# Kernel optimization log

Measured on AMD Instinct MI355X. Metric: run time of the kernel, lower is better.

## Reference

```python
import jax, jax.numpy as jnp
import numpy as np

B, N, M, D, OUT, K = 8, 32, 64, 128, 128, 3
EPS = 1e-5


def batchnorm(x, g, b):
    # training-mode BatchNorm2d over NCHW (stats over B,H,W per channel, biased var)
    mean = x.mean((0, 2, 3), keepdims=True)
    var = ((x - mean) ** 2).mean((0, 2, 3), keepdims=True)
    return g[None, :, None, None] * (x - mean) * jax.lax.rsqrt(var + EPS) + b[None, :, None, None]


def mycorr(x):
    # Pearson correlation between nodes along feature dim: x (B,M,N,D) -> (B,M,N,N)
    xc = x - x.mean(-1, keepdims=True)
    num = jnp.einsum('bmid,bmjd->bmij', xc, xc)
    nrm = jnp.sqrt((xc * xc).sum(-1))
    return num / (nrm[:, :, :, None] * nrm[:, :, None, :] + 1e-8)


def attention(x, W_fc1, W_fc2):
    # x: (B,M,N,D). AdaptiveAvgPool2d((None,1)) over the concat [Wh_i, pos*Wh_j]
    # equals 0.5*(mean_d Wh_i + mean_d(pos*Wh_j)); pos=1 where Wh_i==Wh_j else 2.
    adj = mycorr(x)
    mean_i = x.mean(-1)                       # (B,M,N)
    xi = x[:, :, :, None, :]                  # (B,M,N,1,D)
    xj = x[:, :, None, :, :]                  # (B,M,1,N,D)
    alt_mean = jnp.where(xi == xj, xj, 2.0 * xj).mean(-1)  # (B,M,N,N)
    e = 0.5 * (mean_i[:, :, :, None] + alt_mean)            # (B,M,N,N)
    ef = e.reshape(e.shape[0], e.shape[1], -1)              # (B,M,N*N) pair channels
    h = jax.nn.relu(jnp.einsum('rp,bmp->bmr', W_fc1, ef))
    e2 = jax.nn.sigmoid(jnp.einsum('pr,bmr->bmp', W_fc2, h)).reshape(e.shape)
    att = jax.nn.softmax(jnp.where(adj > 0, e2, jnp.float32(-1e12)), axis=-1)
    return jnp.einsum('bmij,bmjd->bmid', att, x)


def setup_inputs() -> dict:
    key = jax.random.key(0)
    ks = jax.random.split(key, 8)
    P, r, s = N * N, (N * N) // 2, 0.05
    return {
        'x': jax.random.normal(ks[0], (B, N, M, D), jnp.float32),
        'W_sc': jax.random.normal(ks[1], (OUT, M), jnp.float32) * s,
        'g_sc': jnp.ones(OUT, jnp.float32), 'b_sc': jnp.zeros(OUT, jnp.float32),
        'W_l1': jax.random.normal(ks[2], (M, M), jnp.float32) * s,
        'g1': jnp.ones(M, jnp.float32), 'b1': jnp.zeros(M, jnp.float32),
        'W_fc1': jax.random.normal(ks[3], (r, P), jnp.float32) * s,
        'W_fc2': jax.random.normal(ks[4], (P, r), jnp.float32) * s,
        'g2': jnp.ones(M, jnp.float32), 'b2': jnp.zeros(M, jnp.float32),
        'W_dw': jax.random.normal(ks[5], (N, 1, K, K), jnp.float32) * s,
        'g3': jnp.ones(N, jnp.float32), 'b3': jnp.zeros(N, jnp.float32),
        'W_l3': jax.random.normal(ks[6], (OUT, M), jnp.float32) * s,
    }


def reference(x, W_sc, g_sc, b_sc, W_l1, g1, b1, W_fc1, W_fc2, g2, b2, W_dw, g3, b3, W_l3):
    xm = jnp.transpose(x, (0, 2, 1, 3))  # (B,M,N,D)
    # shortcut: 1x1 conv over head channel + BN (stride=1 path)
    shortcut = batchnorm(jnp.einsum('om,bmnd->bond', W_sc, xm), g_sc, b_sc)
    # layer_1: 1x1 conv, BN, global node attention, BN, ReLU
    out = batchnorm(jnp.einsum('cm,bmnd->bcnd', W_l1, xm), g1, b1)
    out = attention(out, W_fc1, W_fc2)
    out = jax.nn.relu(batchnorm(out, g2, b2))
    # layer_2: depthwise KxK conv over (head, dim) per node, BN, ReLU
    out = jnp.transpose(out, (0, 2, 1, 3))  # (B,N,M,D)
    pad = K // 2
    out = jax.lax.conv_general_dilated(out, W_dw, (1, 1), ((pad, pad), (pad, pad)),
                                       feature_group_count=N,
                                       dimension_numbers=('NCHW', 'OIHW', 'NCHW'))
    out = jax.nn.relu(batchnorm(out, g3, b3))
    # layer_3: 1x1 conv to out_channels heads + residual
    out = jnp.transpose(out, (0, 2, 1, 3))  # (B,M,N,D)
    out = jnp.einsum('om,bmnd->bond', W_l3, out) + shortcut
    return jnp.transpose(out, (0, 2, 1, 3))  # (B,N,OUT,D)
```

## Files before the change

### kernel.cpp

```cpp
#include <hip/hip_runtime.h>
#include <math.h>

#define EPS 1e-5f


__device__ __forceinline__ void fma4(float4& a, float s, const float4& v) {
    a.x += s * v.x; a.y += s * v.y; a.z += s * v.z; a.w += s * v.w;
}

__global__ __launch_bounds__(256) void k1_matmul_stats(
    const float* __restrict__ x, const float* __restrict__ Wsc,
    const float* __restrict__ Wl1, const float* __restrict__ Wfc1,
    float* __restrict__ t_sc, float* __restrict__ t_l1,
    float* __restrict__ C1, float* __restrict__ stats)
{
    int g  = blockIdx.x;
    int bn = blockIdx.y;
    __shared__ __align__(16) float s_x[64 * 128];
    __shared__ __align__(16) float s_wT[64 * 68];
    int t = threadIdx.x;

    if (g == 3) {
#pragma unroll
        for (int rr = 0; rr < 2; rr++) {
            int r = bn * 2 + rr;
            *(float4*)(s_x + t * 4) =
                *(const float4*)(Wfc1 + (size_t)r * 1024 + t * 4);
            __syncthreads();
            if (t < 32) {
                float rs = 0.f, cs = 0.f;
#pragma unroll
                for (int j = 0; j < 32; j++) {
                    rs += s_x[t * 32 + j];
                    cs += s_x[j * 32 + t];
                }
                C1[r * 32 + t] = (rs + 2.f * cs - s_x[t * 33]) * (1.0f / 256.0f);
            }
            __syncthreads();
        }
        return;
    }

    int b = bn >> 5, n = bn & 31;
    const float4* xg = (const float4*)(x + (size_t)bn * 8192);
    for (int i = t; i < 2048; i += 256) ((float4*)s_x)[i] = xg[i];

    const float* wbase = (g < 2) ? (Wsc + (size_t)g * 64 * 64) : Wl1;
    for (int i = t; i < 1024; i += 256) {
        int m = i >> 4, rq = (i & 15) * 4;
        float4 wv;
        wv.x = wbase[(size_t)(rq + 0) * 64 + m];
        wv.y = wbase[(size_t)(rq + 1) * 64 + m];
        wv.z = wbase[(size_t)(rq + 2) * 64 + m];
        wv.w = wbase[(size_t)(rq + 3) * 64 + m];
        *(float4*)(s_wT + m * 68 + rq) = wv;
    }
    __syncthreads();

    int wv = t >> 6, lane = t & 63;
    int dl = lane & 15;
    int g4 = lane >> 4;
    int d0 = dl * 8;
    int c0 = wv * 16 + g4 * 4;

    float4 acc[4][2];
#pragma unroll
    for (int i = 0; i < 4; i++) { acc[i][0] = make_float4(0,0,0,0); acc[i][1] = make_float4(0,0,0,0); }

    for (int m = 0; m < 64; m += 2) {
        float4 x00 = *(const float4*)(s_x + m * 128 + d0);
        float4 x01 = *(const float4*)(s_x + m * 128 + d0 + 4);
        float4 x10 = *(const float4*)(s_x + (m + 1) * 128 + d0);
        float4 x11 = *(const float4*)(s_x + (m + 1) * 128 + d0 + 4);
        float4 w0 = *(const float4*)(s_wT + m * 68 + c0);
        float4 w1 = *(const float4*)(s_wT + (m + 1) * 68 + c0);
        fma4(acc[0][0], w0.x, x00); fma4(acc[0][1], w0.x, x01);
        fma4(acc[1][0], w0.y, x00); fma4(acc[1][1], w0.y, x01);
        fma4(acc[2][0], w0.z, x00); fma4(acc[2][1], w0.z, x01);
        fma4(acc[3][0], w0.w, x00); fma4(acc[3][1], w0.w, x01);
        fma4(acc[0][0], w1.x, x10); fma4(acc[0][1], w1.x, x11);
        fma4(acc[1][0], w1.y, x10); fma4(acc[1][1], w1.y, x11);
        fma4(acc[2][0], w1.z, x10); fma4(acc[2][1], w1.z, x11);
        fma4(acc[3][0], w1.w, x10); fma4(acc[3][1], w1.w, x11);
    }

#pragma unroll
    for (int i = 0; i < 4; i++) {
        int cc = g * 64 + c0 + i;
        float4 v0 = acc[i][0], v1 = acc[i][1];
        float* dst;
        if (cc < 128) dst = t_sc + (((size_t)(b * 128 + cc)) * 32 + n) * 128 + d0;
        else          dst = t_l1 + (((size_t)(b * 64 + (cc - 128))) * 32 + n) * 128 + d0;
        *(float4*)dst = v0;
        *(float4*)(dst + 4) = v1;
        float s = v0.x + v0.y + v0.z + v0.w + v1.x + v1.y + v1.z + v1.w;
        float q = v0.x*v0.x + v0.y*v0.y + v0.z*v0.z + v0.w*v0.w
                + v1.x*v1.x + v1.y*v1.y + v1.z*v1.z + v1.w*v1.w;
#pragma unroll
        for (int off = 8; off > 0; off >>= 1) {
            s += __shfl_down(s, off, 16);
            q += __shfl_down(q, off, 16);
        }
        if (dl == 0) {
            if (cc < 128) {
                atomicAdd(&stats[cc], s);
                atomicAdd(&stats[cc + 128], q);
            } else {
                atomicAdd(&stats[256 + (cc - 128)], s);
                atomicAdd(&stats[320 + (cc - 128)], q);
            }
        }
    }
}

__global__ __launch_bounds__(256) void k2_attn_prep(
    const float* __restrict__ t_l1, const float* __restrict__ g1,
    const float* __restrict__ b1, const float* __restrict__ stats,
    const float* __restrict__ Wfc1, const float* __restrict__ C1,
    float* __restrict__ y_g, float* __restrict__ H,
    unsigned int* __restrict__ maskbits)
{
    int bm = blockIdx.x;
    int t  = threadIdx.x;
    __shared__ __align__(16) float y_s[32 * 132];
    __shared__ float S_s[32];
    __shared__ unsigned int m_s[32];
    __shared__ int anom_cnt;
    __shared__ int anom_p[64];
    __shared__ float anom_v[64];
    int m = bm & 63;
    float mean = stats[256 + m] * (1.0f / 32768.0f);
    float var  = stats[320 + m] * (1.0f / 32768.0f) - mean * mean;
    float a = g1[m] * rsqrtf(var + EPS);
    float c = b1[m] - a * mean;

    if (t == 0) anom_cnt = 0;
    if (t < 32) m_s[t] = 0u;
    const float4* src = (const float4*)(t_l1 + (size_t)bm * 4096);
    for (int i = t; i < 1024; i += 256) {
        float4 v = src[i];
        v.x = a * v.x + c; v.y = a * v.y + c; v.z = a * v.z + c; v.w = a * v.w + c;
        int row = i >> 5, col = (i & 31) * 4;
        *(float4*)(y_s + row * 132 + col) = v;
    }
    __syncthreads();

    {
        int r = t >> 3, j = t & 7;
        float s = 0.f;
        const float* yr = y_s + r * 132 + j * 16;
#pragma unroll
        for (int dd = 0; dd < 16; dd++) s += yr[dd];
#pragma unroll
        for (int off = 4; off > 0; off >>= 1) s += __shfl_down(s, off, 8);
        if (j == 0) S_s[r] = s;
    }
    __syncthreads();

    int i = t >> 3, j0 = (t & 7) * 4;
    float dot[4] = {0.f, 0.f, 0.f, 0.f};
    float eqs[4] = {0.f, 0.f, 0.f, 0.f};
    const float* yi = y_s + i * 132;
    for (int dq = 0; dq < 32; dq++) {
        float4 a4 = *(const float4*)(yi + dq * 4);
#pragma unroll
        for (int q = 0; q < 4; q++) {
            float4 b4 = *(const float4*)(y_s + (j0 + q) * 132 + dq * 4);
            dot[q] += a4.x * b4.x + a4.y * b4.y + a4.z * b4.z + a4.w * b4.w;
            eqs[q] += (a4.x == b4.x ? b4.x : 0.f) + (a4.y == b4.y ? b4.y : 0.f)
                    + (a4.z == b4.z ? b4.z : 0.f) + (a4.w == b4.w ? b4.w : 0.f);
        }
    }
    float Si = S_s[i];
    unsigned int bits = 0u;
#pragma unroll
    for (int q = 0; q < 4; q++) {
        int j = j0 + q;
        float Sj = S_s[j];
        float num = dot[q] - Si * Sj * (1.0f / 128.0f);
        if (num > 0.f) bits |= (1u << j);
        if (j != i && eqs[q] != 0.f) {
            int idx = atomicAdd(&anom_cnt, 1);
            if (idx < 64) {
                anom_p[idx] = i * 32 + j;
                anom_v[idx] = eqs[q] * (1.0f / 256.0f);
            }
        }
    }
    atomicOr(&m_s[i], bits);
    __syncthreads();
    if (t < 32) maskbits[bm * 32 + t] = m_s[t];

    int cnt = anom_cnt; if (cnt > 64) cnt = 64;
#pragma unroll
    for (int rr = 0; rr < 2; rr++) {
        int r = t * 2 + rr;
        const float4* c1r = (const float4*)(C1 + r * 32);
        float acc = 0.f;
#pragma unroll
        for (int kk = 0; kk < 8; kk++) {
            float4 cv = c1r[kk];
            acc += cv.x * S_s[kk * 4 + 0] + cv.y * S_s[kk * 4 + 1]
                 + cv.z * S_s[kk * 4 + 2] + cv.w * S_s[kk * 4 + 3];
        }
        for (int a2 = 0; a2 < cnt; a2++)
            acc -= Wfc1[(size_t)r * 1024 + anom_p[a2]] * anom_v[a2];
        H[(size_t)bm * 512 + r] = fmaxf(acc, 0.f);
    }

    float4* yd = (float4*)(y_g + (size_t)bm * 4096);
    for (int idx = t; idx < 1024; idx += 256) {
        int row = idx >> 5, col = (idx & 31) * 4;
        yd[idx] = *(const float4*)(y_s + row * 132 + col);
    }
}

template<int KDIM, int MODE>
__global__ __launch_bounds__(256) void k3_gemm(
    const float* __restrict__ A, const float* __restrict__ Bm,
    float* __restrict__ C, int NC)
{
    __shared__ __align__(16) float lds[4 * 2304];
    int t = threadIdx.x;
    int w = t >> 6, l = t & 63;
    int ct = blockIdx.x, rt = blockIdx.y;
    int row0 = rt * 32, col0 = ct * 32;
    float* As = lds + w * 2304;
    float* Bs = As + 1152;
    int rg = l >> 3;
    int cg = l & 7;
    int kq = (l & 7) * 4;
    constexpr int SLABS = KDIM / 128;

    float4 acc[4];
#pragma unroll
    for (int ii = 0; ii < 4; ii++) acc[ii] = make_float4(0,0,0,0);

    float4 av[4], bv[4], av2[4], bv2[4];
    int k0 = w * 32;
#pragma unroll
    for (int rr = 0; rr < 4; rr++) {
        int r = rg + rr * 8;
        av[rr] = *(const float4*)(A  + (size_t)(row0 + r) * KDIM + k0 + kq);
        bv[rr] = *(const float4*)(Bm + (size_t)(col0 + r) * KDIM + k0 + kq);
    }

    for (int s = 0; s < SLABS; s++) {
#pragma unroll
        for (int rr = 0; rr < 4; rr++) {
            int r = rg + rr * 8;
            As[(kq + 0) * 36 + r] = av[rr].x; As[(kq + 1) * 36 + r] = av[rr].y;
            As[(kq + 2) * 36 + r] = av[rr].z; As[(kq + 3) * 36 + r] = av[rr].w;
            Bs[(kq + 0) * 36 + r] = bv[rr].x; Bs[(kq + 1) * 36 + r] = bv[rr].y;
            Bs[(kq + 2) * 36 + r] = bv[rr].z; Bs[(kq + 3) * 36 + r] = bv[rr].w;
        }
        if (s + 1 < SLABS) {
            int kn = (4 * (s + 1) + w) * 32;
#pragma unroll
            for (int rr = 0; rr < 4; rr++) {
                int r = rg + rr * 8;
                av2[rr] = *(const float4*)(A  + (size_t)(row0 + r) * KDIM + kn + kq);
                bv2[rr] = *(const float4*)(Bm + (size_t)(col0 + r) * KDIM + kn + kq);
            }
        }
#pragma unroll
        for (int k = 0; k < 32; k++) {
            float4 a = *(const float4*)(As + k * 36 + rg * 4);
            float4 b = *(const float4*)(Bs + k * 36 + cg * 4);
            fma4(acc[0], a.x, b);
            fma4(acc[1], a.y, b);
            fma4(acc[2], a.z, b);
            fma4(acc[3], a.w, b);
        }
#pragma unroll
        for (int rr = 0; rr < 4; rr++) { av[rr] = av2[rr]; bv[rr] = bv2[rr]; }
    }

    __syncthreads();
    float* red = lds;
#pragma unroll
    for (int ii = 0; ii < 4; ii++)
        *(float4*)(red + w * 1024 + (rg * 4 + ii) * 32 + cg * 4) = acc[ii];
    __syncthreads();

    int r = t >> 3, c4 = (t & 7) * 4;
    float4 s0 = *(const float4*)(red + r * 32 + c4);
    float4 s1 = *(const float4*)(red + 1024 + r * 32 + c4);
    float4 s2 = *(const float4*)(red + 2048 + r * 32 + c4);
    float4 s3 = *(const float4*)(red + 3072 + r * 32 + c4);
    float4 v;
    v.x = s0.x + s1.x + s2.x + s3.x;
    v.y = s0.y + s1.y + s2.y + s3.y;
    v.z = s0.z + s1.z + s2.z + s3.z;
    v.w = s0.w + s1.w + s2.w + s3.w;
    if (MODE == 0) {
        v.x = fmaxf(v.x, 0.f); v.y = fmaxf(v.y, 0.f);
        v.z = fmaxf(v.z, 0.f); v.w = fmaxf(v.w, 0.f);
    } else {
        v.x = 1.0f / (1.0f + expf(-v.x)); v.y = 1.0f / (1.0f + expf(-v.y));
        v.z = 1.0f / (1.0f + expf(-v.z)); v.w = 1.0f / (1.0f + expf(-v.w));
    }
    *(float4*)(C + (size_t)(row0 + r) * NC + col0 + c4) = v;
}

__global__ __launch_bounds__(256) void k4_attn_apply(
    const float* __restrict__ E2, const unsigned int* __restrict__ maskbits,
    const float* __restrict__ y_g, float* __restrict__ att_out,
    float* __restrict__ stats)
{
    int bm = blockIdx.x;
    int t  = threadIdx.x;
    __shared__ __align__(16) float att_s[32 * 33];
    __shared__ __align__(16) float y_sh[32 * 128];
    __shared__ float redS[4], redQ[4];

    const float4* ysrc = (const float4*)(y_g + (size_t)bm * 4096);
    float4* yds = (float4*)y_sh;
    for (int i = t; i < 1024; i += 256) yds[i] = ysrc[i];

    {
        int r = t >> 3, j0 = (t & 7) * 4;
        unsigned int mk = maskbits[bm * 32 + r];
        float4 e4 = *(const float4*)(E2 + (size_t)bm * 1024 + r * 32 + j0);
        float v0 = ((mk >> (j0 + 0)) & 1u) ? e4.x : -1e12f;
        float v1 = ((mk >> (j0 + 1)) & 1u) ? e4.y : -1e12f;
        float v2 = ((mk >> (j0 + 2)) & 1u) ? e4.z : -1e12f;
        float v3 = ((mk >> (j0 + 3)) & 1u) ? e4.w : -1e12f;
        float mx = fmaxf(fmaxf(v0, v1), fmaxf(v2, v3));
#pragma unroll
        for (int off = 1; off < 8; off <<= 1) mx = fmaxf(mx, __shfl_xor(mx, off, 8));
        float e0 = __expf(v0 - mx), e1 = __expf(v1 - mx);
        float e2 = __expf(v2 - mx), e3 = __expf(v3 - mx);
        float s = e0 + e1 + e2 + e3;
#pragma unroll
        for (int off = 1; off < 8; off <<= 1) s += __shfl_xor(s, off, 8);
        float inv = 1.0f / s;
        att_s[r * 33 + j0 + 0] = e0 * inv;
        att_s[r * 33 + j0 + 1] = e1 * inv;
        att_s[r * 33 + j0 + 2] = e2 * inv;
        att_s[r * 33 + j0 + 3] = e3 * inv;
    }
    __syncthreads();

    int tx = t & 31, ty = t >> 5;
    int dq = tx * 4;
    int i0 = ty * 4;
    float4 acc0 = make_float4(0,0,0,0), acc1 = make_float4(0,0,0,0);
    float4 acc2 = make_float4(0,0,0,0), acc3 = make_float4(0,0,0,0);
    for (int j = 0; j < 32; j++) {
        float4 yv = *(const float4*)(y_sh + j * 128 + dq);
        float w0 = att_s[(i0 + 0) * 33 + j];
        float w1 = att_s[(i0 + 1) * 33 + j];
        float w2 = att_s[(i0 + 2) * 33 + j];
        float w3 = att_s[(i0 + 3) * 33 + j];
        fma4(acc0, w0, yv);
        fma4(acc1, w1, yv);
        fma4(acc2, w2, yv);
        fma4(acc3, w3, yv);
    }
    float ssum = 0.f, sq = 0.f;
    float4 accs[4] = {acc0, acc1, acc2, acc3};
#pragma unroll
    for (int ii = 0; ii < 4; ii++) {
        float4 acc = accs[ii];
        *(float4*)(att_out + (size_t)bm * 4096 + (i0 + ii) * 128 + dq) = acc;
        ssum += acc.x + acc.y + acc.z + acc.w;
        sq   += acc.x * acc.x + acc.y * acc.y + acc.z * acc.z + acc.w * acc.w;
    }
#pragma unroll
    for (int off = 32; off > 0; off >>= 1) {
        ssum += __shfl_down(ssum, off, 64);
        sq   += __shfl_down(sq, off, 64);
    }
    int wave = t >> 6, lane = t & 63;
    if (lane == 0) { redS[wave] = ssum; redQ[wave] = sq; }
    __syncthreads();
    if (t == 0) {
        float S = redS[0] + redS[1] + redS[2] + redS[3];
        float Q = redQ[0] + redQ[1] + redQ[2] + redQ[3];
        int m = bm & 63;
        atomicAdd(&stats[384 + m], S);
        atomicAdd(&stats[448 + m], Q);
    }
}

__global__ __launch_bounds__(256) void k5_conv(
    const float* __restrict__ att_out, const float* __restrict__ Wdw,
    const float* __restrict__ g2, const float* __restrict__ b2,
    float* __restrict__ stats, float* __restrict__ v_g)
{
    int bn = blockIdx.x;
    int b = bn >> 5, n = bn & 31;
    int t = threadIdx.x;
    __shared__ __align__(16) float z_s[66 * 130];
    __shared__ float a2_s[64], c2_s[64];
    __shared__ float redS[4], redQ[4];

    if (t < 64) {
        float mean = stats[384 + t] * (1.0f / 32768.0f);
        float var  = stats[448 + t] * (1.0f / 32768.0f) - mean * mean;
        float a = g2[t] * rsqrtf(var + EPS);
        a2_s[t] = a; c2_s[t] = b2[t] - a * mean;
    }
    for (int i = t; i < 66 * 130; i += 256) z_s[i] = 0.f;
    __syncthreads();

    for (int i = t; i < 2048; i += 256) {
        int m = i >> 5, c4 = (i & 31) * 4;
        float4 vv = *(const float4*)(att_out + (((size_t)(b * 64 + m)) * 32 + n) * 128 + c4);
        float a = a2_s[m], c = c2_s[m];
        float* dst = z_s + (m + 1) * 130 + c4 + 1;
        dst[0] = fmaxf(a * vv.x + c, 0.f);
        dst[1] = fmaxf(a * vv.y + c, 0.f);
        dst[2] = fmaxf(a * vv.z + c, 0.f);
        dst[3] = fmaxf(a * vv.w + c, 0.f);
    }
    float w[9];
#pragma unroll
    for (int i = 0; i < 9; i++) w[i] = Wdw[n * 9 + i];
    __syncthreads();

    int tx = t & 31, ty = t >> 5;
    int d0 = tx * 4;
    float ssum = 0.f, sq = 0.f;
#pragma unroll
    for (int rr = 0; rr < 8; rr++) {
        int h = ty * 8 + rr;
        float o0 = 0.f, o1 = 0.f, o2 = 0.f, o3 = 0.f;
#pragma unroll
        for (int dh = 0; dh < 3; dh++) {
            const float* zr = z_s + (h + dh) * 130 + d0;
#pragma unroll
            for (int dw = 0; dw < 3; dw++) {
                float wv = w[dh * 3 + dw];
                o0 += wv * zr[dw + 0];
                o1 += wv * zr[dw + 1];
                o2 += wv * zr[dw + 2];
                o3 += wv * zr[dw + 3];
            }
        }
        *(float4*)(v_g + ((size_t)bn * 64 + h) * 128 + d0) = make_float4(o0, o1, o2, o3);
        ssum += o0 + o1 + o2 + o3;
        sq   += o0 * o0 + o1 * o1 + o2 * o2 + o3 * o3;
    }
#pragma unroll
    for (int off = 32; off > 0; off >>= 1) {
        ssum += __shfl_down(ssum, off, 64);
        sq   += __shfl_down(sq, off, 64);
    }
    int wave = t >> 6, lane = t & 63;
    if (lane == 0) { redS[wave] = ssum; redQ[wave] = sq; }
    __syncthreads();
    if (t == 0) {
        atomicAdd(&stats[512 + n], redS[0] + redS[1] + redS[2] + redS[3]);
        atomicAdd(&stats[544 + n], redQ[0] + redQ[1] + redQ[2] + redQ[3]);
    }
}

__global__ __launch_bounds__(256) void k6_final(
    const float* __restrict__ v_g, const float* __restrict__ t_sc,
    const float* __restrict__ Wl3, const float* __restrict__ g3,
    const float* __restrict__ b3, const float* __restrict__ gsc,
    const float* __restrict__ bsc, const float* __restrict__ stats,
    float* __restrict__ outp)
{
    int oh = blockIdx.x;
    int bn = blockIdx.y;
    int b = bn >> 5, n = bn & 31;
    int t = threadIdx.x;
    __shared__ __align__(16) float z_s[64 * 128];
    __shared__ __align__(16) float s_wT[64 * 68];

    float mean3 = stats[512 + n] * (1.0f / 65536.0f);
    float var3  = stats[544 + n] * (1.0f / 65536.0f) - mean3 * mean3;
    float a3 = g3[n] * rsqrtf(var3 + EPS);
    float c3 = b3[n] - a3 * mean3;

    const float4* vsrc = (const float4*)(v_g + (size_t)bn * 8192);
    for (int i = t; i < 2048; i += 256) {
        float4 vv = vsrc[i];
        float4 r;
        r.x = fmaxf(a3 * vv.x + c3, 0.f);
        r.y = fmaxf(a3 * vv.y + c3, 0.f);
        r.z = fmaxf(a3 * vv.z + c3, 0.f);
        r.w = fmaxf(a3 * vv.w + c3, 0.f);
        ((float4*)z_s)[i] = r;
    }
    const float* wbase = Wl3 + (size_t)oh * 64 * 64;
    for (int i = t; i < 1024; i += 256) {
        int m = i >> 4, rq = (i & 15) * 4;
        float4 wv;
        wv.x = wbase[(size_t)(rq + 0) * 64 + m];
        wv.y = wbase[(size_t)(rq + 1) * 64 + m];
        wv.z = wbase[(size_t)(rq + 2) * 64 + m];
        wv.w = wbase[(size_t)(rq + 3) * 64 + m];
        *(float4*)(s_wT + m * 68 + rq) = wv;
    }
    __syncthreads();

    int wv = t >> 6, lane = t & 63;
    int dl = lane & 15, g4 = lane >> 4;
    int d0 = dl * 8;
    int c0 = wv * 16 + g4 * 4;

    float4 acc[4][2];
#pragma unroll
    for (int i = 0; i < 4; i++) { acc[i][0] = make_float4(0,0,0,0); acc[i][1] = make_float4(0,0,0,0); }

    for (int m = 0; m < 64; m += 2) {
        float4 x00 = *(const float4*)(z_s + m * 128 + d0);
        float4 x01 = *(const float4*)(z_s + m * 128 + d0 + 4);
        float4 x10 = *(const float4*)(z_s + (m + 1) * 128 + d0);
        float4 x11 = *(const float4*)(z_s + (m + 1) * 128 + d0 + 4);
        float4 w0 = *(const float4*)(s_wT + m * 68 + c0);
        float4 w1 = *(const float4*)(s_wT + (m + 1) * 68 + c0);
        fma4(acc[0][0], w0.x, x00); fma4(acc[0][1], w0.x, x01);
        fma4(acc[1][0], w0.y, x00); fma4(acc[1][1], w0.y, x01);
        fma4(acc[2][0], w0.z, x00); fma4(acc[2][1], w0.z, x01);
        fma4(acc[3][0], w0.w, x00); fma4(acc[3][1], w0.w, x01);
        fma4(acc[0][0], w1.x, x10); fma4(acc[0][1], w1.x, x11);
        fma4(acc[1][0], w1.y, x10); fma4(acc[1][1], w1.y, x11);
        fma4(acc[2][0], w1.z, x10); fma4(acc[2][1], w1.z, x11);
        fma4(acc[3][0], w1.w, x10); fma4(acc[3][1], w1.w, x11);
    }

#pragma unroll
    for (int i = 0; i < 4; i++) {
        int o = oh * 64 + c0 + i;
        float msc = stats[o] * (1.0f / 32768.0f);
        float vsc = stats[128 + o] * (1.0f / 32768.0f) - msc * msc;
        float asc = gsc[o] * rsqrtf(vsc + EPS);
        float csc = bsc[o] - asc * msc;
        const float* ts = t_sc + (((size_t)(b * 128 + o)) * 32 + n) * 128 + d0;
        float4 t0 = *(const float4*)(ts);
        float4 t1 = *(const float4*)(ts + 4);
        float4 o0 = acc[i][0], o1 = acc[i][1];
        o0.x += asc * t0.x + csc; o0.y += asc * t0.y + csc;
        o0.z += asc * t0.z + csc; o0.w += asc * t0.w + csc;
        o1.x += asc * t1.x + csc; o1.y += asc * t1.y + csc;
        o1.z += asc * t1.z + csc; o1.w += asc * t1.w + csc;
        float* dst = outp + (((size_t)(b * 32 + n)) * 128 + o) * 128 + d0;
        *(float4*)dst = o0;
        *(float4*)(dst + 4) = o1;
    }
}

extern "C" void kernel_launch(void* const* d_in, const int* in_sizes, int n_in,
                              void* d_out, int out_size, void* d_ws, size_t ws_size,
                              hipStream_t stream)
{
    const float* x    = (const float*)d_in[0];
    const float* Wsc  = (const float*)d_in[1];
    const float* gsc  = (const float*)d_in[2];
    const float* bsc  = (const float*)d_in[3];
    const float* Wl1  = (const float*)d_in[4];
    const float* g1   = (const float*)d_in[5];
    const float* b1   = (const float*)d_in[6];
    const float* Wfc1 = (const float*)d_in[7];
    const float* Wfc2 = (const float*)d_in[8];
    const float* g2   = (const float*)d_in[9];
    const float* b2   = (const float*)d_in[10];
    const float* Wdw  = (const float*)d_in[11];
    const float* g3   = (const float*)d_in[12];
    const float* b3   = (const float*)d_in[13];
    const float* Wl3  = (const float*)d_in[14];
    float* outp = (float*)d_out;

    float* ws = (float*)d_ws;
    float* stats = ws;
    float* t_sc  = ws + 1024;
    float* t_l1  = t_sc + 4194304;
    float* y_g   = t_l1 + 2097152;
    float* C1    = y_g + 2097152;
    float* H     = C1 + 16384;
    float* E2    = H + 262144;
    unsigned int* maskb = (unsigned int*)(E2 + 524288);

    (void)hipMemsetAsync(stats, 0, 1024 * sizeof(float), stream);

    k1_matmul_stats<<<dim3(4, 256), 256, 0, stream>>>(x, Wsc, Wl1, Wfc1, t_sc, t_l1, C1, stats);
    k2_attn_prep<<<512, 256, 0, stream>>>(t_l1, g1, b1, stats, Wfc1, C1, y_g, H, maskb);
    k3_gemm<512, 1><<<dim3(32, 16), 256, 0, stream>>>(H, Wfc2, E2, 1024);
    k4_attn_apply<<<512, 256, 0, stream>>>(E2, maskb, y_g, t_l1, stats);
    k5_conv<<<256, 256, 0, stream>>>(t_l1, Wdw, g2, b2, stats, y_g);
    k6_final<<<dim3(2, 256), 256, 0, stream>>>(y_g, t_sc, Wl3, g3, b3, gsc, bsc, stats, outp);
}
```

Measured before the change: 198.8 us.

## Retile 1x1-conv kernels with split-K register tiles and padded shared layouts

The k1 and k6 1x1-conv GEMMs now give each thread an 8-channel by 8-element register tile. The 64-wide reduction is split across two wave pairs, and the halves are combined through shared memory before the epilogue. The x/z and attention y tiles get padded shared-memory strides to cut bank conflicts, and weight transposition loads are restructured to coalesce. The point is to raise FMA-to-LDS ratio and reduce bank conflicts. The cost is higher register pressure (launch_bounds 256,3), an extra shared-memory reduction with two syncs, and half the waves idle in the epilogue.

```diff
diff --git a/kernel.cpp b/kernel.cpp
--- a/kernel.cpp
+++ b/kernel.cpp
@@ -8,7 +8,17 @@
     a.x += s * v.x; a.y += s * v.y; a.z += s * v.z; a.w += s * v.w;
 }
 
-__global__ __launch_bounds__(256) void k1_matmul_stats(
+#define FMA_STEP(W0, W1, X0, X1) \
+    fma4(acc[0][0], W0.x, X0); fma4(acc[0][1], W0.x, X1); \
+    fma4(acc[1][0], W0.y, X0); fma4(acc[1][1], W0.y, X1); \
+    fma4(acc[2][0], W0.z, X0); fma4(acc[2][1], W0.z, X1); \
+    fma4(acc[3][0], W0.w, X0); fma4(acc[3][1], W0.w, X1); \
+    fma4(acc[4][0], W1.x, X0); fma4(acc[4][1], W1.x, X1); \
+    fma4(acc[5][0], W1.y, X0); fma4(acc[5][1], W1.y, X1); \
+    fma4(acc[6][0], W1.z, X0); fma4(acc[6][1], W1.z, X1); \
+    fma4(acc[7][0], W1.w, X0); fma4(acc[7][1], W1.w, X1);
+
+__global__ __launch_bounds__(256, 3) void k1_matmul_stats(
     const float* __restrict__ x, const float* __restrict__ Wsc,
     const float* __restrict__ Wl1, const float* __restrict__ Wfc1,
     float* __restrict__ t_sc, float* __restrict__ t_l1,
@@ -16,7 +26,7 @@
 {
     int g  = blockIdx.x;
     int bn = blockIdx.y;
-    __shared__ __align__(16) float s_x[64 * 128];
+    __shared__ __align__(16) float s_x[64 * 144];
     __shared__ __align__(16) float s_wT[64 * 68];
     int t = threadIdx.x;
 
@@ -43,75 +53,108 @@
 
     int b = bn >> 5, n = bn & 31;
     const float4* xg = (const float4*)(x + (size_t)bn * 8192);
-    for (int i = t; i < 2048; i += 256) ((float4*)s_x)[i] = xg[i];
-
-    const float* wbase = (g < 2) ? (Wsc + (size_t)g * 64 * 64) : Wl1;
-    for (int i = t; i < 1024; i += 256) {
-        int m = i >> 4, rq = (i & 15) * 4;
-        float4 wv;
-        wv.x = wbase[(size_t)(rq + 0) * 64 + m];
-        wv.y = wbase[(size_t)(rq + 1) * 64 + m];
-        wv.z = wbase[(size_t)(rq + 2) * 64 + m];
-        wv.w = wbase[(size_t)(rq + 3) * 64 + m];
-        *(float4*)(s_wT + m * 68 + rq) = wv;
-    }
-    __syncthreads();
-
-    int wv = t >> 6, lane = t & 63;
-    int dl = lane & 15;
-    int g4 = lane >> 4;
+    for (int i = t; i < 2048; i += 256) {
+        int row = i >> 5, j = i & 31;
+        *(float4*)(s_x + row * 144 + j * 4 + ((j >> 3) << 2)) = xg[i];
+    }
+    const float* wbase = (g < 2) ? (Wsc + (size_t)g * 4096) : Wl1;
+    {
+        int m = t & 63, tg = t >> 6;
+        float val[16];
+#pragma unroll
+        for (int o = 0; o < 16; o++)
+            val[o] = wbase[(size_t)(tg * 16 + o) * 64 + m];
+        float* wr = s_wT + m * 68 + tg * 16;
+#pragma unroll
+        for (int q = 0; q < 8; q++)
+            *(float2*)(wr + 2 * q) = make_float2(val[2 * q], val[2 * q + 1]);
+    }
+    __syncthreads();
+
+    int w = t >> 6, lane = t & 63;
+    int mh = w >> 1, p = w & 1;
+    int dl = lane & 15, cg = lane >> 4;
     int d0 = dl * 8;
-    int c0 = wv * 16 + g4 * 4;
-
-    float4 acc[4][2];
-#pragma unroll
-    for (int i = 0; i < 4; i++) { acc[i][0] = make_float4(0,0,0,0); acc[i][1] = make_float4(0,0,0,0); }
-
-    for (int m = 0; m < 64; m += 2) {
-        float4 x00 = *(const float4*)(s_x + m * 128 + d0);
-        float4 x01 = *(const float4*)(s_x + m * 128 + d0 + 4);
-        float4 x10 = *(const float4*)(s_x + (m + 1) * 128 + d0);
-        float4 x11 = *(const float4*)(s_x + (m + 1) * 128 + d0 + 4);
-        float4 w0 = *(const float4*)(s_wT + m * 68 + c0);
-        float4 w1 = *(const float4*)(s_wT + (m + 1) * 68 + c0);
-        fma4(acc[0][0], w0.x, x00); fma4(acc[0][1], w0.x, x01);
-        fma4(acc[1][0], w0.y, x00); fma4(acc[1][1], w0.y, x01);
-        fma4(acc[2][0], w0.z, x00); fma4(acc[2][1], w0.z, x01);
-        fma4(acc[3][0], w0.w, x00); fma4(acc[3][1], w0.w, x01);
-        fma4(acc[0][0], w1.x, x10); fma4(acc[0][1], w1.x, x11);
-        fma4(acc[1][0], w1.y, x10); fma4(acc[1][1], w1.y, x11);
-        fma4(acc[2][0], w1.z, x10); fma4(acc[2][1], w1.z, x11);
-        fma4(acc[3][0], w1.w, x10); fma4(acc[3][1], w1.w, x11);
-    }
-
-#pragma unroll
-    for (int i = 0; i < 4; i++) {
-        int cc = g * 64 + c0 + i;
-        float4 v0 = acc[i][0], v1 = acc[i][1];
-        float* dst;
-        if (cc < 128) dst = t_sc + (((size_t)(b * 128 + cc)) * 32 + n) * 128 + d0;
-        else          dst = t_l1 + (((size_t)(b * 64 + (cc - 128))) * 32 + n) * 128 + d0;
-        *(float4*)dst = v0;
-        *(float4*)(dst + 4) = v1;
-        float s = v0.x + v0.y + v0.z + v0.w + v1.x + v1.y + v1.z + v1.w;
-        float q = v0.x*v0.x + v0.y*v0.y + v0.z*v0.z + v0.w*v0.w
-                + v1.x*v1.x + v1.y*v1.y + v1.z*v1.z + v1.w*v1.w;
-#pragma unroll
-        for (int off = 8; off > 0; off >>= 1) {
-            s += __shfl_down(s, off, 16);
-            q += __shfl_down(q, off, 16);
-        }
-        if (dl == 0) {
-            if (cc < 128) {
-                atomicAdd(&stats[cc], s);
-                atomicAdd(&stats[cc + 128], q);
-            } else {
-                atomicAdd(&stats[256 + (cc - 128)], s);
-                atomicAdd(&stats[320 + (cc - 128)], q);
+    int ch = p * 32 + cg * 8;
+    int xoff = d0 + ((dl >> 2) << 2);
+
+    float4 acc[8][2];
+#pragma unroll
+    for (int i = 0; i < 8; i++) { acc[i][0] = make_float4(0,0,0,0); acc[i][1] = make_float4(0,0,0,0); }
+
+    int m0 = mh * 32;
+    for (int m = m0; m < m0 + 32; m += 2) {
+        const float* xr0 = s_x + m * 144 + xoff;
+        const float* wr0 = s_wT + m * 68 + ch;
+        float4 xA0 = *(const float4*)(xr0);
+        float4 xA1 = *(const float4*)(xr0 + 4);
+        float4 xB0 = *(const float4*)(xr0 + 144);
+        float4 xB1 = *(const float4*)(xr0 + 148);
+        float4 wA0 = *(const float4*)(wr0);
+        float4 wA1 = *(const float4*)(wr0 + 4);
+        float4 wB0 = *(const float4*)(wr0 + 68);
+        float4 wB1 = *(const float4*)(wr0 + 72);
+        FMA_STEP(wA0, wA1, xA0, xA1)
+        FMA_STEP(wB0, wB1, xB0, xB1)
+    }
+
+    __syncthreads();
+    float* s_red = s_x;
+    if (mh == 1) {
+        float* row = s_red + (p * 64 + lane) * 66;
+#pragma unroll
+        for (int i = 0; i < 8; i++) {
+            *(float2*)(row + i * 8 + 0) = make_float2(acc[i][0].x, acc[i][0].y);
+            *(float2*)(row + i * 8 + 2) = make_float2(acc[i][0].z, acc[i][0].w);
+            *(float2*)(row + i * 8 + 4) = make_float2(acc[i][1].x, acc[i][1].y);
+            *(float2*)(row + i * 8 + 6) = make_float2(acc[i][1].z, acc[i][1].w);
+        }
+    }
+    __syncthreads();
+    if (mh == 0) {
+        const float* row = s_red + (p * 64 + lane) * 66;
+#pragma unroll
+        for (int i = 0; i < 8; i++) {
+            float2 p0 = *(const float2*)(row + i * 8 + 0);
+            float2 p1 = *(const float2*)(row + i * 8 + 2);
+            float2 p2 = *(const float2*)(row + i * 8 + 4);
+            float2 p3 = *(const float2*)(row + i * 8 + 6);
+            acc[i][0].x += p0.x; acc[i][0].y += p0.y;
+            acc[i][0].z += p1.x; acc[i][0].w += p1.y;
+            acc[i][1].x += p2.x; acc[i][1].y += p2.y;
+            acc[i][1].z += p3.x; acc[i][1].w += p3.y;
+        }
+#pragma unroll
+        for (int i = 0; i < 8; i++) {
+            int cc = g * 64 + ch + i;
+            float4 v0 = acc[i][0], v1 = acc[i][1];
+            float* dst;
+            if (cc < 128) dst = t_sc + (((size_t)(b * 128 + cc)) * 32 + n) * 128 + d0;
+            else          dst = t_l1 + (((size_t)(b * 64 + (cc - 128))) * 32 + n) * 128 + d0;
+            *(float4*)dst = v0;
+            *(float4*)(dst + 4) = v1;
+            float s = v0.x + v0.y + v0.z + v0.w + v1.x + v1.y + v1.z + v1.w;
+            float q = v0.x*v0.x + v0.y*v0.y + v0.z*v0.z + v0.w*v0.w
+                    + v1.x*v1.x + v1.y*v1.y + v1.z*v1.z + v1.w*v1.w;
+#pragma unroll
+            for (int off = 8; off > 0; off >>= 1) {
+                s += __shfl_down(s, off, 16);
+                q += __shfl_down(q, off, 16);
             }
-        }
-    }
-}
+            if (dl == 0) {
+                if (cc < 128) {
+                    atomicAdd(&stats[cc], s);
+                    atomicAdd(&stats[cc + 128], q);
+                } else {
+                    atomicAdd(&stats[256 + (cc - 128)], s);
+                    atomicAdd(&stats[320 + (cc - 128)], q);
+                }
+            }
+        }
+    }
+}
+
+__device__ __forceinline__ int yb(int r) { return r * 132 + ((r >> 2) << 3); }
 
 __global__ __launch_bounds__(256) void k2_attn_prep(
     const float* __restrict__ t_l1, const float* __restrict__ g1,
@@ -122,7 +165,7 @@
 {
     int bm = blockIdx.x;
     int t  = threadIdx.x;
-    __shared__ __align__(16) float y_s[32 * 132];
+    __shared__ __align__(16) float y_s[4288];
     __shared__ float S_s[32];
     __shared__ unsigned int m_s[32];
     __shared__ int anom_cnt;
@@ -141,14 +184,14 @@
         float4 v = src[i];
         v.x = a * v.x + c; v.y = a * v.y + c; v.z = a * v.z + c; v.w = a * v.w + c;
         int row = i >> 5, col = (i & 31) * 4;
-        *(float4*)(y_s + row * 132 + col) = v;
+        *(float4*)(y_s + yb(row) + col) = v;
     }
     __syncthreads();
 
     {
         int r = t >> 3, j = t & 7;
         float s = 0.f;
-        const float* yr = y_s + r * 132 + j * 16;
+        const float* yr = y_s + yb(r) + j * 16;
 #pragma unroll
         for (int dd = 0; dd < 16; dd++) s += yr[dd];
 #pragma unroll
@@ -160,12 +203,14 @@
     int i = t >> 3, j0 = (t & 7) * 4;
     float dot[4] = {0.f, 0.f, 0.f, 0.f};
     float eqs[4] = {0.f, 0.f, 0.f, 0.f};
-    const float* yi = y_s + i * 132;
+    const float* yi = y_s + yb(i);
+    const float* yj[4] = { y_s + yb(j0), y_s + yb(j0 + 1),
+                           y_s + yb(j0 + 2), y_s + yb(j0 + 3) };
     for (int dq = 0; dq < 32; dq++) {
         float4 a4 = *(const float4*)(yi + dq * 4);
 #pragma unroll
         for (int q = 0; q < 4; q++) {
-            float4 b4 = *(const float4*)(y_s + (j0 + q) * 132 + dq * 4);
+            float4 b4 = *(const float4*)(yj[q] + dq * 4);
             dot[q] += a4.x * b4.x + a4.y * b4.y + a4.z * b4.z + a4.w * b4.w;
             eqs[q] += (a4.x == b4.x ? b4.x : 0.f) + (a4.y == b4.y ? b4.y : 0.f)
                     + (a4.z == b4.z ? b4.z : 0.f) + (a4.w == b4.w ? b4.w : 0.f);
@@ -211,7 +256,7 @@
     float4* yd = (float4*)(y_g + (size_t)bm * 4096);
     for (int idx = t; idx < 1024; idx += 256) {
         int row = idx >> 5, col = (idx & 31) * 4;
-        yd[idx] = *(const float4*)(y_s + row * 132 + col);
+        yd[idx] = *(const float4*)(y_s + yb(row) + col);
     }
 }
 
@@ -457,7 +502,7 @@
     }
 }
 
-__global__ __launch_bounds__(256) void k6_final(
+__global__ __launch_bounds__(256, 3) void k6_final(
     const float* __restrict__ v_g, const float* __restrict__ t_sc,
     const float* __restrict__ Wl3, const float* __restrict__ g3,
     const float* __restrict__ b3, const float* __restrict__ gsc,
@@ -468,7 +513,7 @@
     int bn = blockIdx.y;
     int b = bn >> 5, n = bn & 31;
     int t = threadIdx.x;
-    __shared__ __align__(16) float z_s[64 * 128];
+    __shared__ __align__(16) float z_s[64 * 144];
     __shared__ __align__(16) float s_wT[64 * 68];
 
     float mean3 = stats[512 + n] * (1.0f / 65536.0f);
@@ -484,64 +529,95 @@
         r.y = fmaxf(a3 * vv.y + c3, 0.f);
         r.z = fmaxf(a3 * vv.z + c3, 0.f);
         r.w = fmaxf(a3 * vv.w + c3, 0.f);
-        ((float4*)z_s)[i] = r;
-    }
-    const float* wbase = Wl3 + (size_t)oh * 64 * 64;
-    for (int i = t; i < 1024; i += 256) {
-        int m = i >> 4, rq = (i & 15) * 4;
-        float4 wv;
-        wv.x = wbase[(size_t)(rq + 0) * 64 + m];
-        wv.y = wbase[(size_t)(rq + 1) * 64 + m];
-        wv.z = wbase[(size_t)(rq + 2) * 64 + m];
-        wv.w = wbase[(size_t)(rq + 3) * 64 + m];
-        *(float4*)(s_wT + m * 68 + rq) = wv;
-    }
-    __syncthreads();
-
-    int wv = t >> 6, lane = t & 63;
-    int dl = lane & 15, g4 = lane >> 4;
+        int row = i >> 5, j = i & 31;
+        *(float4*)(z_s + row * 144 + j * 4 + ((j >> 3) << 2)) = r;
+    }
+    const float* wbase = Wl3 + (size_t)oh * 4096;
+    {
+        int m = t & 63, tg = t >> 6;
+        float val[16];
+#pragma unroll
+        for (int o = 0; o < 16; o++)
+            val[o] = wbase[(size_t)(tg * 16 + o) * 64 + m];
+        float* wr = s_wT + m * 68 + tg * 16;
+#pragma unroll
+        for (int q = 0; q < 8; q++)
+            *(float2*)(wr + 2 * q) = make_float2(val[2 * q], val[2 * q + 1]);
+    }
+    __syncthreads();
+
+    int w = t >> 6, lane = t & 63;
+    int mh = w >> 1, p = w & 1;
+    int dl = lane & 15, cg = lane >> 4;
     int d0 = dl * 8;
-    int c0 = wv * 16 + g4 * 4;
-
-    float4 acc[4][2];
-#pragma unroll
-    for (int i = 0; i < 4; i++) { acc[i][0] = make_float4(0,0,0,0); acc[i][1] = make_float4(0,0,0,0); }
-
-    for (int m = 0; m < 64; m += 2) {
-        float4 x00 = *(const float4*)(z_s + m * 128 + d0);
-        float4 x01 = *(const float4*)(z_s + m * 128 + d0 + 4);
-        float4 x10 = *(const float4*)(z_s + (m + 1) * 128 + d0);
-        float4 x11 = *(const float4*)(z_s + (m + 1) * 128 + d0 + 4);
-        float4 w0 = *(const float4*)(s_wT + m * 68 + c0);
-        float4 w1 = *(const float4*)(s_wT + (m + 1) * 68 + c0);
-        fma4(acc[0][0], w0.x, x00); fma4(acc[0][1], w0.x, x01);
-        fma4(acc[1][0], w0.y, x00); fma4(acc[1][1], w0.y, x01);
-        fma4(acc[2][0], w0.z, x00); fma4(acc[2][1], w0.z, x01);
-        fma4(acc[3][0], w0.w, x00); fma4(acc[3][1], w0.w, x01);
-        fma4(acc[0][0], w1.x, x10); fma4(acc[0][1], w1.x, x11);
-        fma4(acc[1][0], w1.y, x10); fma4(acc[1][1], w1.y, x11);
-        fma4(acc[2][0], w1.z, x10); fma4(acc[2][1], w1.z, x11);
-        fma4(acc[3][0], w1.w, x10); fma4(acc[3][1], w1.w, x11);
-    }
-
-#pragma unroll
-    for (int i = 0; i < 4; i++) {
-        int o = oh * 64 + c0 + i;
-        float msc = stats[o] * (1.0f / 32768.0f);
-        float vsc = stats[128 + o] * (1.0f / 32768.0f) - msc * msc;
-        float asc = gsc[o] * rsqrtf(vsc + EPS);
-        float csc = bsc[o] - asc * msc;
-        const float* ts = t_sc + (((size_t)(b * 128 + o)) * 32 + n) * 128 + d0;
-        float4 t0 = *(const float4*)(ts);
-        float4 t1 = *(const float4*)(ts + 4);
-        float4 o0 = acc[i][0], o1 = acc[i][1];
-        o0.x += asc * t0.x + csc; o0.y += asc * t0.y + csc;
-        o0.z += asc * t0.z + csc; o0.w += asc * t0.w + csc;
-        o1.x += asc * t1.x + csc; o1.y += asc * t1.y + csc;
-        o1.z += asc * t1.z + csc; o1.w += asc * t1.w + csc;
-        float* dst = outp + (((size_t)(b * 32 + n)) * 128 + o) * 128 + d0;
-        *(float4*)dst = o0;
-        *(float4*)(dst + 4) = o1;
+    int ch = p * 32 + cg * 8;
+    int xoff = d0 + ((dl >> 2) << 2);
+
+    float4 acc[8][2];
+#pragma unroll
+    for (int i = 0; i < 8; i++) { acc[i][0] = make_float4(0,0,0,0); acc[i][1] = make_float4(0,0,0,0); }
+
+    int m0 = mh * 32;
+    for (int m = m0; m < m0 + 32; m += 2) {
+        const float* xr0 = z_s + m * 144 + xoff;
+        const float* wr0 = s_wT + m * 68 + ch;
+        float4 xA0 = *(const float4*)(xr0);
+        float4 xA1 = *(const float4*)(xr0 + 4);
+        float4 xB0 = *(const float4*)(xr0 + 144);
+        float4 xB1 = *(const float4*)(xr0 + 148);
+        float4 wA0 = *(const float4*)(wr0);
+        float4 wA1 = *(const float4*)(wr0 + 4);
+        float4 wB0 = *(const float4*)(wr0 + 68);
+        float4 wB1 = *(const float4*)(wr0 + 72);
+        FMA_STEP(wA0, wA1, xA0, xA1)
+        FMA_STEP(wB0, wB1, xB0, xB1)
+    }
+
+    __syncthreads();
+    float* s_red = z_s;
+    if (mh == 1) {
+        float* row = s_red + (p * 64 + lane) * 66;
+#pragma unroll
+        for (int i = 0; i < 8; i++) {
+            *(float2*)(row + i * 8 + 0) = make_float2(acc[i][0].x, acc[i][0].y);
+            *(float2*)(row + i * 8 + 2) = make_float2(acc[i][0].z, acc[i][0].w);
+            *(float2*)(row + i * 8 + 4) = make_float2(acc[i][1].x, acc[i][1].y);
+            *(float2*)(row + i * 8 + 6) = make_float2(acc[i][1].z, acc[i][1].w);
+        }
+    }
+    __syncthreads();
+    if (mh == 0) {
+        const float* row = s_red + (p * 64 + lane) * 66;
+#pragma unroll
+        for (int i = 0; i < 8; i++) {
+            float2 p0 = *(const float2*)(row + i * 8 + 0);
+            float2 p1 = *(const float2*)(row + i * 8 + 2);
+            float2 p2 = *(const float2*)(row + i * 8 + 4);
+            float2 p3 = *(const float2*)(row + i * 8 + 6);
+            acc[i][0].x += p0.x; acc[i][0].y += p0.y;
+            acc[i][0].z += p1.x; acc[i][0].w += p1.y;
+            acc[i][1].x += p2.x; acc[i][1].y += p2.y;
+            acc[i][1].z += p3.x; acc[i][1].w += p3.y;
+        }
+#pragma unroll
+        for (int i = 0; i < 8; i++) {
+            int o = oh * 64 + ch + i;
+            float msc = stats[o] * (1.0f / 32768.0f);
+            float vsc = stats[128 + o] * (1.0f / 32768.0f) - msc * msc;
+            float asc = gsc[o] * rsqrtf(vsc + EPS);
+            float csc = bsc[o] - asc * msc;
+            const float* ts = t_sc + (((size_t)(b * 128 + o)) * 32 + n) * 128 + d0;
+            float4 t0 = *(const float4*)(ts);
+            float4 t1 = *(const float4*)(ts + 4);
+            float4 o0 = acc[i][0], o1 = acc[i][1];
+            o0.x += asc * t0.x + csc; o0.y += asc * t0.y + csc;
+            o0.z += asc * t0.z + csc; o0.w += asc * t0.w + csc;
+            o1.x += asc * t1.x + csc; o1.y += asc * t1.y + csc;
+            o1.z += asc * t1.z + csc; o1.w += asc * t1.w + csc;
+            float* dst = outp + (((size_t)(b * 32 + n)) * 128 + o) * 128 + d0;
+            *(float4*)dst = o0;
+            *(float4*)(dst + 4) = o1;
+        }
     }
 }
 
```

Result: slower. 213.6 us (+7.5%).

## Pre-transpose 1x1-conv weights once and pad shared tiles to avoid bank conflicts

Applied to the files above, without the earlier changes.

Adds a small kernel that transposes the shortcut, layer-1 and layer-3 1x1-conv weights into global buffers once per call. k1 and k6 then read weights straight from global/L2 instead of each block doing strided transposes into shared memory, which cuts LDS use and allows four blocks per CU via launch bounds. Shared activation tiles get padded row strides and swizzle offsets in k1, k2 and k6 to reduce LDS bank conflicts, and the inner loops are unrolled. This costs an extra kernel launch and moves the weight reads into the inner loop, where they now hit cache rather than LDS.

```diff
diff --git a/kernel.cpp b/kernel.cpp
--- a/kernel.cpp
+++ b/kernel.cpp
@@ -8,16 +8,32 @@
     a.x += s * v.x; a.y += s * v.y; a.z += s * v.z; a.w += s * v.w;
 }
 
-__global__ __launch_bounds__(256) void k1_matmul_stats(
-    const float* __restrict__ x, const float* __restrict__ Wsc,
-    const float* __restrict__ Wl1, const float* __restrict__ Wfc1,
-    float* __restrict__ t_sc, float* __restrict__ t_l1,
-    float* __restrict__ C1, float* __restrict__ stats)
+__global__ __launch_bounds__(256) void k0_transpose(
+    const float* __restrict__ Wsc, const float* __restrict__ Wl1,
+    const float* __restrict__ Wl3, float* __restrict__ Wt,
+    float* __restrict__ Wt3)
+{
+    int idx = blockIdx.x * 256 + threadIdx.x;
+    if (idx < 12288) {
+        int m = idx / 192, cc = idx % 192;
+        Wt[idx] = (cc < 128) ? Wsc[(size_t)cc * 64 + m]
+                             : Wl1[(size_t)(cc - 128) * 64 + m];
+    } else if (idx < 20480) {
+        int k = idx - 12288;
+        int m = k >> 7, o = k & 127;
+        Wt3[k] = Wl3[(size_t)o * 64 + m];
+    }
+}
+
+__global__ __launch_bounds__(256, 4) void k1_matmul_stats(
+    const float* __restrict__ x, const float* __restrict__ Wt,
+    const float* __restrict__ Wfc1, float* __restrict__ t_sc,
+    float* __restrict__ t_l1, float* __restrict__ C1,
+    float* __restrict__ stats)
 {
     int g  = blockIdx.x;
     int bn = blockIdx.y;
-    __shared__ __align__(16) float s_x[64 * 128];
-    __shared__ __align__(16) float s_wT[64 * 68];
+    __shared__ __align__(16) float s_x[64 * 144];
     int t = threadIdx.x;
 
     if (g == 3) {
@@ -43,37 +59,32 @@
 
     int b = bn >> 5, n = bn & 31;
     const float4* xg = (const float4*)(x + (size_t)bn * 8192);
-    for (int i = t; i < 2048; i += 256) ((float4*)s_x)[i] = xg[i];
-
-    const float* wbase = (g < 2) ? (Wsc + (size_t)g * 64 * 64) : Wl1;
-    for (int i = t; i < 1024; i += 256) {
-        int m = i >> 4, rq = (i & 15) * 4;
-        float4 wv;
-        wv.x = wbase[(size_t)(rq + 0) * 64 + m];
-        wv.y = wbase[(size_t)(rq + 1) * 64 + m];
-        wv.z = wbase[(size_t)(rq + 2) * 64 + m];
-        wv.w = wbase[(size_t)(rq + 3) * 64 + m];
-        *(float4*)(s_wT + m * 68 + rq) = wv;
+    for (int i = t; i < 2048; i += 256) {
+        int row = i >> 5, j = i & 31;
+        *(float4*)(s_x + row * 144 + j * 4 + ((j >> 3) << 2)) = xg[i];
     }
     __syncthreads();
 
     int wv = t >> 6, lane = t & 63;
-    int dl = lane & 15;
-    int g4 = lane >> 4;
+    int dl = lane & 15, g4 = lane >> 4;
     int d0 = dl * 8;
     int c0 = wv * 16 + g4 * 4;
+    int xoff = d0 + ((dl >> 2) << 2);
+    const float* wt = Wt + g * 64 + c0;
 
     float4 acc[4][2];
 #pragma unroll
     for (int i = 0; i < 4; i++) { acc[i][0] = make_float4(0,0,0,0); acc[i][1] = make_float4(0,0,0,0); }
 
+#pragma unroll 4
     for (int m = 0; m < 64; m += 2) {
-        float4 x00 = *(const float4*)(s_x + m * 128 + d0);
-        float4 x01 = *(const float4*)(s_x + m * 128 + d0 + 4);
-        float4 x10 = *(const float4*)(s_x + (m + 1) * 128 + d0);
-        float4 x11 = *(const float4*)(s_x + (m + 1) * 128 + d0 + 4);
-        float4 w0 = *(const float4*)(s_wT + m * 68 + c0);
-        float4 w1 = *(const float4*)(s_wT + (m + 1) * 68 + c0);
+        const float* xr = s_x + m * 144 + xoff;
+        float4 x00 = *(const float4*)(xr);
+        float4 x01 = *(const float4*)(xr + 4);
+        float4 x10 = *(const float4*)(xr + 144);
+        float4 x11 = *(const float4*)(xr + 148);
+        float4 w0 = *(const float4*)(wt + m * 192);
+        float4 w1 = *(const float4*)(wt + (m + 1) * 192);
         fma4(acc[0][0], w0.x, x00); fma4(acc[0][1], w0.x, x01);
         fma4(acc[1][0], w0.y, x00); fma4(acc[1][1], w0.y, x01);
         fma4(acc[2][0], w0.z, x00); fma4(acc[2][1], w0.z, x01);
@@ -113,6 +124,8 @@
     }
 }
 
+__device__ __forceinline__ int yb(int r) { return r * 132 + ((r >> 2) << 3); }
+
 __global__ __launch_bounds__(256) void k2_attn_prep(
     const float* __restrict__ t_l1, const float* __restrict__ g1,
     const float* __restrict__ b1, const float* __restrict__ stats,
@@ -122,7 +135,7 @@
 {
     int bm = blockIdx.x;
     int t  = threadIdx.x;
-    __shared__ __align__(16) float y_s[32 * 132];
+    __shared__ __align__(16) float y_s[4288];
     __shared__ float S_s[32];
     __shared__ unsigned int m_s[32];
     __shared__ int anom_cnt;
@@ -141,14 +154,14 @@
         float4 v = src[i];
         v.x = a * v.x + c; v.y = a * v.y + c; v.z = a * v.z + c; v.w = a * v.w + c;
         int row = i >> 5, col = (i & 31) * 4;
-        *(float4*)(y_s + row * 132 + col) = v;
+        *(float4*)(y_s + yb(row) + col) = v;
     }
     __syncthreads();
 
     {
         int r = t >> 3, j = t & 7;
         float s = 0.f;
-        const float* yr = y_s + r * 132 + j * 16;
+        const float* yr = y_s + yb(r) + j * 16;
 #pragma unroll
         for (int dd = 0; dd < 16; dd++) s += yr[dd];
 #pragma unroll
@@ -160,12 +173,14 @@
     int i = t >> 3, j0 = (t & 7) * 4;
     float dot[4] = {0.f, 0.f, 0.f, 0.f};
     float eqs[4] = {0.f, 0.f, 0.f, 0.f};
-    const float* yi = y_s + i * 132;
+    const float* yi = y_s + yb(i);
+    const float* yj[4] = { y_s + yb(j0), y_s + yb(j0 + 1),
+                           y_s + yb(j0 + 2), y_s + yb(j0 + 3) };
     for (int dq = 0; dq < 32; dq++) {
         float4 a4 = *(const float4*)(yi + dq * 4);
 #pragma unroll
         for (int q = 0; q < 4; q++) {
-            float4 b4 = *(const float4*)(y_s + (j0 + q) * 132 + dq * 4);
+            float4 b4 = *(const float4*)(yj[q] + dq * 4);
             dot[q] += a4.x * b4.x + a4.y * b4.y + a4.z * b4.z + a4.w * b4.w;
             eqs[q] += (a4.x == b4.x ? b4.x : 0.f) + (a4.y == b4.y ? b4.y : 0.f)
                     + (a4.z == b4.z ? b4.z : 0.f) + (a4.w == b4.w ? b4.w : 0.f);
@@ -211,7 +226,7 @@
     float4* yd = (float4*)(y_g + (size_t)bm * 4096);
     for (int idx = t; idx < 1024; idx += 256) {
         int row = idx >> 5, col = (idx & 31) * 4;
-        yd[idx] = *(const float4*)(y_s + row * 132 + col);
+        yd[idx] = *(const float4*)(y_s + yb(row) + col);
     }
 }
 
@@ -457,9 +472,9 @@
     }
 }
 
-__global__ __launch_bounds__(256) void k6_final(
+__global__ __launch_bounds__(256, 4) void k6_final(
     const float* __restrict__ v_g, const float* __restrict__ t_sc,
-    const float* __restrict__ Wl3, const float* __restrict__ g3,
+    const float* __restrict__ Wt3, const float* __restrict__ g3,
     const float* __restrict__ b3, const float* __restrict__ gsc,
     const float* __restrict__ bsc, const float* __restrict__ stats,
     float* __restrict__ outp)
@@ -468,8 +483,7 @@
     int bn = blockIdx.y;
     int b = bn >> 5, n = bn & 31;
     int t = threadIdx.x;
-    __shared__ __align__(16) float z_s[64 * 128];
-    __shared__ __align__(16) float s_wT[64 * 68];
+    __shared__ __align__(16) float z_s[64 * 144];
 
     float mean3 = stats[512 + n] * (1.0f / 65536.0f);
     float var3  = stats[544 + n] * (1.0f / 65536.0f) - mean3 * mean3;
@@ -484,17 +498,8 @@
         r.y = fmaxf(a3 * vv.y + c3, 0.f);
         r.z = fmaxf(a3 * vv.z + c3, 0.f);
         r.w = fmaxf(a3 * vv.w + c3, 0.f);
-        ((float4*)z_s)[i] = r;
-    }
-    const float* wbase = Wl3 + (size_t)oh * 64 * 64;
-    for (int i = t; i < 1024; i += 256) {
-        int m = i >> 4, rq = (i & 15) * 4;
-        float4 wv;
-        wv.x = wbase[(size_t)(rq + 0) * 64 + m];
-        wv.y = wbase[(size_t)(rq + 1) * 64 + m];
-        wv.z = wbase[(size_t)(rq + 2) * 64 + m];
-        wv.w = wbase[(size_t)(rq + 3) * 64 + m];
-        *(float4*)(s_wT + m * 68 + rq) = wv;
+        int row = i >> 5, j = i & 31;
+        *(float4*)(z_s + row * 144 + j * 4 + ((j >> 3) << 2)) = r;
     }
     __syncthreads();
 
@@ -502,18 +507,22 @@
     int dl = lane & 15, g4 = lane >> 4;
     int d0 = dl * 8;
     int c0 = wv * 16 + g4 * 4;
+    int xoff = d0 + ((dl >> 2) << 2);
+    const float* wt = Wt3 + oh * 64 + c0;
 
     float4 acc[4][2];
 #pragma unroll
     for (int i = 0; i < 4; i++) { acc[i][0] = make_float4(0,0,0,0); acc[i][1] = make_float4(0,0,0,0); }
 
+#pragma unroll 4
     for (int m = 0; m < 64; m += 2) {
-        float4 x00 = *(const float4*)(z_s + m * 128 + d0);
-        float4 x01 = *(const float4*)(z_s + m * 128 + d0 + 4);
-        float4 x10 = *(const float4*)(z_s + (m + 1) * 128 + d0);
-        float4 x11 = *(const float4*)(z_s + (m + 1) * 128 + d0 + 4);
-        float4 w0 = *(const float4*)(s_wT + m * 68 + c0);
-        float4 w1 = *(const float4*)(s_wT + (m + 1) * 68 + c0);
+        const float* xr = z_s + m * 144 + xoff;
+        float4 x00 = *(const float4*)(xr);
+        float4 x01 = *(const float4*)(xr + 4);
+        float4 x10 = *(const float4*)(xr + 144);
+        float4 x11 = *(const float4*)(xr + 148);
+        float4 w0 = *(const float4*)(wt + m * 128);
+        float4 w1 = *(const float4*)(wt + (m + 1) * 128);
         fma4(acc[0][0], w0.x, x00); fma4(acc[0][1], w0.x, x01);
         fma4(acc[1][0], w0.y, x00); fma4(acc[1][1], w0.y, x01);
         fma4(acc[2][0], w0.z, x00); fma4(acc[2][1], w0.z, x01);
@@ -575,13 +584,16 @@
     float* H     = C1 + 16384;
     float* E2    = H + 262144;
     unsigned int* maskb = (unsigned int*)(E2 + 524288);
+    float* Wt    = (float*)(maskb + 16384);
+    float* Wt3   = Wt + 12288;
 
     (void)hipMemsetAsync(stats, 0, 1024 * sizeof(float), stream);
 
-    k1_matmul_stats<<<dim3(4, 256), 256, 0, stream>>>(x, Wsc, Wl1, Wfc1, t_sc, t_l1, C1, stats);
+    k0_transpose<<<80, 256, 0, stream>>>(Wsc, Wl1, Wl3, Wt, Wt3);
+    k1_matmul_stats<<<dim3(4, 256), 256, 0, stream>>>(x, Wt, Wfc1, t_sc, t_l1, C1, stats);
     k2_attn_prep<<<512, 256, 0, stream>>>(t_l1, g1, b1, stats, Wfc1, C1, y_g, H, maskb);
     k3_gemm<512, 1><<<dim3(32, 16), 256, 0, stream>>>(H, Wfc2, E2, 1024);
     k4_attn_apply<<<512, 256, 0, stream>>>(E2, maskb, y_g, t_l1, stats);
     k5_conv<<<256, 256, 0, stream>>>(t_l1, Wdw, g2, b2, stats, y_g);
-    k6_final<<<dim3(2, 256), 256, 0, stream>>>(y_g, t_sc, Wl3, g3, b3, gsc, bsc, stats, outp);
-}
+    k6_final<<<dim3(2, 256), 256, 0, stream>>>(y_g, t_sc, Wt3, g3, b3, gsc, bsc, stats, outp);
+}
```

New measurement: 194.7 us. -2.1%, faster.
